# Performance work log

Measured on AMD Instinct MI355X. Metric: run time of the kernel, lower is better.

Reference implementation:

```python
import jax, jax.numpy as jnp
import numpy as np

N = 262144   # faces = edges = vertices
E = 2000000  # connections per bipartite edge set
W = 32       # out_width


def _linear_block(x, w, b):
    # LinearBlock(in, out) with defaults -> Linear + LeakyReLU(0.01)
    return jax.nn.leaky_relu(x @ w + b)


def _bip_res_mr_conv(x_src, x_dst, e, w, b):
    # diffs = x_dst[e1] - x_src[e0]; scatter_max over dst; MLP(cat) residual
    diffs = x_dst[e[1]] - x_src[e[0]]                       # [E, W]
    maxes = jax.ops.segment_max(diffs, e[1], num_segments=x_dst.shape[0])
    # torch_scatter.scatter_max fills empty slots with 0
    maxes = jnp.where(jnp.isfinite(maxes), maxes, 0.0)
    h = _linear_block(jnp.concatenate([x_dst, maxes], axis=1), w, b)
    return x_dst + h


def setup_inputs() -> dict:
    key = jax.random.key(0)
    ks = jax.random.split(key, 16)
    inp = {
        "x_f": jax.random.normal(ks[0], (N, 4), dtype=jnp.float32),
        "x_e": jax.random.normal(ks[1], (N, 6), dtype=jnp.float32),
        "x_v": jax.random.normal(ks[2], (N, 3), dtype=jnp.float32),
        "e_fe": jax.random.randint(ks[3], (2, E), 0, N),
        "e_ev": jax.random.randint(ks[4], (2, E), 0, N),
        "e_ef": jax.random.randint(ks[5], (2, E), 0, N),
        "e_ve": jax.random.randint(ks[6], (2, E), 0, N),
    }
    def lin(k, cin, cout):
        s = 1.0 / np.sqrt(cin)
        kw, kb = jax.random.split(k)
        return (jax.random.uniform(kw, (cin, cout), minval=-s, maxval=s, dtype=jnp.float32),
                jax.random.uniform(kb, (cout,), minval=-s, maxval=s, dtype=jnp.float32))
    inp["wf"], inp["bf"] = lin(ks[7], 4, W)
    inp["we"], inp["be"] = lin(ks[8], 6, W)
    inp["wv"], inp["bv"] = lin(ks[9], 3, W)
    inp["w_f2e"], inp["b_f2e"] = lin(ks[10], 2 * W, W)
    inp["w_e2v"], inp["b_e2v"] = lin(ks[11], 2 * W, W)   # E2V conv
    return inp


def reference(x_f, x_e, x_v, e_fe, e_ev, e_ef, e_ve,
              wf, bf, we, be, wv, bv, w_f2e, b_f2e, w_e2v, b_e2v):
    x_f = _linear_block(x_f, wf, bf)
    x_e = _linear_block(x_e, we, be)
    x_v = _linear_block(x_v, wv, bv)
    # NB: original forward reuses self.F2E weights for three convs
    x_e = _bip_res_mr_conv(x_f, x_e, e_fe, w_f2e, b_f2e)
    x_v = _bip_res_mr_conv(x_e, x_v, e_ev, w_e2v, b_e2v)
    x_f = _bip_res_mr_conv(x_e, x_f, e_ef, w_f2e, b_f2e)
    x_e = _bip_res_mr_conv(x_v, x_e, e_ve, w_f2e, b_f2e)
    return (x_f, x_e, x_v)
```

## Files before the change

kernel.cpp:

```cpp
#include <hip/hip_runtime.h>
#include <math.h>

#define N_NODES 262144
#define NE      2000000
#define W_OUT   32

#define NBINS          2048
#define BIN_SHIFT      7
#define NODES_PER_BIN  128
#define CAP            1200
#define EPT            16

__device__ __forceinline__ float lrelu(float x) { return x >= 0.f ? x : 0.01f * x; }

__device__ __forceinline__ unsigned fmin_key(float f) {
    unsigned u = __float_as_uint(f);
    return (u & 0x80000000u) ? ~u : (u | 0x80000000u);
}
__device__ __forceinline__ float fmin_unkey(unsigned u) {
    return __uint_as_float((u & 0x80000000u) ? (u ^ 0x80000000u) : ~u);
}

template<int K>
__global__ void proj_kernel(const float* __restrict__ x, const float* __restrict__ w,
                            const float* __restrict__ b, float* __restrict__ out) {
    __shared__ float wl[K * 32];
    __shared__ float xl[8 * K];
    int t = threadIdx.x;
    for (int i = t; i < K * 32; i += 256) wl[i] = w[i];
    int nbase = blockIdx.x * 8;
    for (int i = t; i < 8 * K; i += 256) xl[i] = x[nbase * K + i];
    __syncthreads();
    int j = t & 31, ln = t >> 5;
    float acc = b[j];
#pragma unroll
    for (int k = 0; k < K; ++k) acc += xl[ln * K + k] * wl[k * 32 + j];
    out[nbase * 32 + t] = lrelu(acc);
}

__global__ void bin_pass(const int* __restrict__ e0, const int* __restrict__ e1,
                         int* __restrict__ gcur, unsigned int* __restrict__ buckets) {
    __shared__ unsigned int hist[NBINS];
    __shared__ unsigned int lcur[NBINS];
    __shared__ unsigned int gbase[NBINS];
    int t = threadIdx.x;
    for (int i = t; i < NBINS; i += 256) hist[i] = 0;
    __syncthreads();
    long base = (long)blockIdx.x * (256 * EPT);
    for (int k = 0; k < EPT; ++k) {
        long i = base + k * 256 + t;
        if (i < NE) atomicAdd(&hist[((unsigned)e1[i]) >> BIN_SHIFT], 1u);
    }
    __syncthreads();
    for (int i = t; i < NBINS; i += 256) {
        gbase[i] = atomicAdd((unsigned int*)&gcur[i], hist[i]);
        lcur[i] = 0;
    }
    __syncthreads();
    for (int k = 0; k < EPT; ++k) {
        long i = base + k * 256 + t;
        if (i < NE) {
            unsigned d = (unsigned)e1[i];
            unsigned s = (unsigned)e0[i];
            unsigned bin = d >> BIN_SHIFT;
            unsigned pos = gbase[bin] + atomicAdd(&lcur[bin], 1u);
            if (pos < CAP)
                buckets[(size_t)bin * CAP + pos] =
                    ((d & (NODES_PER_BIN - 1u)) << 18) | s;
        }
    }
}

__global__ __launch_bounds__(256)
void binreduce4(const int* __restrict__ gcur, const unsigned int* __restrict__ buckets,
                const float* __restrict__ src, const float* __restrict__ dst,
                const float* __restrict__ w, const float* __restrict__ b,
                float* __restrict__ out) {
    __shared__ unsigned int mxu[(NODES_PER_BIN + 1) * 32];
    __shared__ float wl[64 * 32];
    __shared__ __align__(16) float xmat[8][4][64];
    int t = threadIdx.x;
    int bin = blockIdx.x;
    int hw = t >> 5, c = t & 31;

    uint4* m4 = (uint4*)mxu;
    for (int i = t; i < (NODES_PER_BIN + 1) * 32 / 4; i += 256)
        m4[i] = make_uint4(0xFFFFFFFFu, 0xFFFFFFFFu, 0xFFFFFFFFu, 0xFFFFFFFFu);
    for (int i = t; i < 64 * 32; i += 256) wl[i] = w[i];
    __syncthreads();

    int nb = min(gcur[bin], CAP);
    const unsigned int* bk = buckets + (size_t)bin * CAP;
    const unsigned SENT = (unsigned)NODES_PER_BIN << 18;
    for (int cbase = hw * 32; cbase < nb; cbase += 256) {
        int idx = cbase + c;
        unsigned ent = (idx < nb) ? bk[idx] : SENT;
#pragma unroll
        for (int k0 = 0; k0 < 32; k0 += 8) {
            float v[8];
            unsigned nd[8];
#pragma unroll
            for (int j = 0; j < 8; ++j) {
                unsigned e = __shfl(ent, k0 + j, 32);
                nd[j] = e >> 18;
                v[j] = src[(size_t)(e & 0x3FFFFu) * 32 + c];
            }
#pragma unroll
            for (int j = 0; j < 8; ++j)
                atomicMin(&mxu[nd[j] * 32 + c], fmin_key(v[j]));
        }
    }
    __syncthreads();

    float bc = b[c];
    size_t gb = (size_t)bin * NODES_PER_BIN;
    for (int grp = 0; grp < 4; ++grp) {
        int n0 = hw * 16 + grp * 4;
#pragma unroll
        for (int g = 0; g < 4; ++g) {
            int node = n0 + g;
            float dv = dst[(gb + node) * 32 + c];
            unsigned mu = mxu[node * 32 + c];
            float mx = (mu == 0xFFFFFFFFu) ? 0.0f : (dv - fmin_unkey(mu));
            xmat[hw][g][c] = dv;
            xmat[hw][g][32 + c] = mx;
        }
        __threadfence_block();

        float acc[4];
#pragma unroll
        for (int g = 0; g < 4; ++g) acc[g] = bc;

#pragma unroll 4
        for (int k4 = 0; k4 < 16; ++k4) {
            float w0 = wl[(k4 * 4 + 0) * 32 + c];
            float w1 = wl[(k4 * 4 + 1) * 32 + c];
            float w2 = wl[(k4 * 4 + 2) * 32 + c];
            float w3 = wl[(k4 * 4 + 3) * 32 + c];
#pragma unroll
            for (int g = 0; g < 4; ++g) {
                float4 xv = ((const float4*)xmat[hw][g])[k4];
                acc[g] += xv.x * w0 + xv.y * w1 + xv.z * w2 + xv.w * w3;
            }
        }
#pragma unroll
        for (int g = 0; g < 4; ++g) {
            float dv = xmat[hw][g][c];
            out[(gb + n0 + g) * 32 + c] = dv + lrelu(acc[g]);
        }
        __threadfence_block();
    }
}

extern "C" void kernel_launch(void* const* d_in, const int* in_sizes, int n_in,
                              void* d_out, int out_size, void* d_ws, size_t ws_size,
                              hipStream_t stream) {
    const float* x_f  = (const float*)d_in[0];
    const float* x_e  = (const float*)d_in[1];
    const float* x_v  = (const float*)d_in[2];
    const int*   e_fe = (const int*)d_in[3];
    const int*   e_ev = (const int*)d_in[4];
    const int*   e_ef = (const int*)d_in[5];
    const int*   e_ve = (const int*)d_in[6];
    const float* wf    = (const float*)d_in[7];
    const float* bf    = (const float*)d_in[8];
    const float* we    = (const float*)d_in[9];
    const float* be    = (const float*)d_in[10];
    const float* wv    = (const float*)d_in[11];
    const float* bv    = (const float*)d_in[12];
    const float* w_f2e = (const float*)d_in[13];
    const float* b_f2e = (const float*)d_in[14];
    const float* w_e2v = (const float*)d_in[15];
    const float* b_e2v = (const float*)d_in[16];

    float* of = (float*)d_out;
    float* oe = of + (size_t)N_NODES * W_OUT;
    float* ov = oe + (size_t)N_NODES * W_OUT;

    const int NW = N_NODES * W_OUT;

    float*        xe1     = (float*)d_ws;
    unsigned int* buckets = (unsigned int*)(xe1 + NW);
    int*          gcur4   = (int*)(buckets + (size_t)NBINS * CAP);

    dim3 blk(256);
    const int bgrid = (NE + 256 * EPT - 1) / (256 * EPT);

    hipMemsetAsync(gcur4, 0, 4 * NBINS * sizeof(int), stream);

    proj_kernel<4><<<N_NODES / 8, blk, 0, stream>>>(x_f, wf, bf, of);
    proj_kernel<6><<<N_NODES / 8, blk, 0, stream>>>(x_e, we, be, oe);
    proj_kernel<3><<<N_NODES / 8, blk, 0, stream>>>(x_v, wv, bv, ov);

    int conv_id = 0;
    auto conv = [&](const float* src, const float* dstb, const int* e,
                    const float* w, const float* bias, float* out) {
        int* gcur = gcur4 + conv_id * NBINS;
        ++conv_id;
        bin_pass<<<bgrid, blk, 0, stream>>>(e, e + NE, gcur, buckets);
        binreduce4<<<NBINS, blk, 0, stream>>>(gcur, buckets, src, dstb, w, bias, out);
    };

    conv(of,  oe,  e_fe, w_f2e, b_f2e, xe1);
    conv(xe1, ov,  e_ev, w_e2v, b_e2v, ov);
    conv(xe1, of,  e_ef, w_f2e, b_f2e, of);
    conv(ov,  xe1, e_ve, w_f2e, b_f2e, oe);
}
```

Before: 509.3 us.

## Vectorize edge binning loads and gather src rows as float4 with padded LDS

The binning pass now reads edge indices as int4, four per thread per step, in place of scalar loads. The reduce kernel uses 64-lane wavefronts: 8 lanes cooperatively gather one 128-byte src row as float4. The shared max table is padded to 33 words per row to cut LDS bank conflicts on the atomicMin updates. The MLP epilogue processes 2 nodes per group instead of 4, which lowers register use. In exchange, each lane issues four LDS atomics per load, and within a bin the order in which edges are bucketed changes.

```diff
diff --git a/kernel.cpp b/kernel.cpp
--- a/kernel.cpp
+++ b/kernel.cpp
@@ -9,7 +9,8 @@
 #define BIN_SHIFT      7
 #define NODES_PER_BIN  128
 #define CAP            1200
-#define EPT            16
+#define MROW           33
+#define MXU_DW         (((NODES_PER_BIN + 1) * MROW + 3) & ~3)
 
 __device__ __forceinline__ float lrelu(float x) { return x >= 0.f ? x : 0.01f * x; }
 
@@ -38,18 +39,28 @@
     out[nbase * 32 + t] = lrelu(acc);
 }
 
-__global__ void bin_pass(const int* __restrict__ e0, const int* __restrict__ e1,
-                         int* __restrict__ gcur, unsigned int* __restrict__ buckets) {
+__global__ __launch_bounds__(256)
+void bin_pass2(const int* __restrict__ e0, const int* __restrict__ e1,
+               int* __restrict__ gcur, unsigned int* __restrict__ buckets) {
     __shared__ unsigned int hist[NBINS];
     __shared__ unsigned int lcur[NBINS];
     __shared__ unsigned int gbase[NBINS];
     int t = threadIdx.x;
     for (int i = t; i < NBINS; i += 256) hist[i] = 0;
     __syncthreads();
-    long base = (long)blockIdx.x * (256 * EPT);
-    for (int k = 0; k < EPT; ++k) {
-        long i = base + k * 256 + t;
-        if (i < NE) atomicAdd(&hist[((unsigned)e1[i]) >> BIN_SHIFT], 1u);
+
+    int q0 = blockIdx.x * 1024 + t;
+    int4 d4[4];
+#pragma unroll
+    for (int k = 0; k < 4; ++k) {
+        int q = q0 + k * 256;
+        if (q * 4 < NE) {
+            d4[k] = ((const int4*)e1)[q];
+            atomicAdd(&hist[((unsigned)d4[k].x) >> BIN_SHIFT], 1u);
+            atomicAdd(&hist[((unsigned)d4[k].y) >> BIN_SHIFT], 1u);
+            atomicAdd(&hist[((unsigned)d4[k].z) >> BIN_SHIFT], 1u);
+            atomicAdd(&hist[((unsigned)d4[k].w) >> BIN_SHIFT], 1u);
+        }
     }
     __syncthreads();
     for (int i = t; i < NBINS; i += 256) {
@@ -57,34 +68,39 @@
         lcur[i] = 0;
     }
     __syncthreads();
-    for (int k = 0; k < EPT; ++k) {
-        long i = base + k * 256 + t;
-        if (i < NE) {
-            unsigned d = (unsigned)e1[i];
-            unsigned s = (unsigned)e0[i];
-            unsigned bin = d >> BIN_SHIFT;
-            unsigned pos = gbase[bin] + atomicAdd(&lcur[bin], 1u);
-            if (pos < CAP)
-                buckets[(size_t)bin * CAP + pos] =
-                    ((d & (NODES_PER_BIN - 1u)) << 18) | s;
+#pragma unroll
+    for (int k = 0; k < 4; ++k) {
+        int q = q0 + k * 256;
+        if (q * 4 < NE) {
+            int4 s4 = ((const int4*)e0)[q];
+            const int ds[4] = {d4[k].x, d4[k].y, d4[k].z, d4[k].w};
+            const int ss[4] = {s4.x, s4.y, s4.z, s4.w};
+#pragma unroll
+            for (int j = 0; j < 4; ++j) {
+                unsigned d = (unsigned)ds[j];
+                unsigned bin = d >> BIN_SHIFT;
+                unsigned pos = gbase[bin] + atomicAdd(&lcur[bin], 1u);
+                if (pos < CAP)
+                    buckets[(size_t)bin * CAP + pos] =
+                        ((d & (NODES_PER_BIN - 1u)) << 18) | (unsigned)ss[j];
+            }
         }
     }
 }
 
 __global__ __launch_bounds__(256)
-void binreduce4(const int* __restrict__ gcur, const unsigned int* __restrict__ buckets,
+void binreduce5(const int* __restrict__ gcur, const unsigned int* __restrict__ buckets,
                 const float* __restrict__ src, const float* __restrict__ dst,
                 const float* __restrict__ w, const float* __restrict__ b,
                 float* __restrict__ out) {
-    __shared__ unsigned int mxu[(NODES_PER_BIN + 1) * 32];
+    __shared__ unsigned int mxu[MXU_DW];
     __shared__ float wl[64 * 32];
-    __shared__ __align__(16) float xmat[8][4][64];
+    __shared__ __align__(16) float xmat[8][2][64];
     int t = threadIdx.x;
     int bin = blockIdx.x;
-    int hw = t >> 5, c = t & 31;
 
     uint4* m4 = (uint4*)mxu;
-    for (int i = t; i < (NODES_PER_BIN + 1) * 32 / 4; i += 256)
+    for (int i = t; i < MXU_DW / 4; i += 256)
         m4[i] = make_uint4(0xFFFFFFFFu, 0xFFFFFFFFu, 0xFFFFFFFFu, 0xFFFFFFFFu);
     for (int i = t; i < 64 * 32; i += 256) wl[i] = w[i];
     __syncthreads();
@@ -92,62 +108,57 @@
     int nb = min(gcur[bin], CAP);
     const unsigned int* bk = buckets + (size_t)bin * CAP;
     const unsigned SENT = (unsigned)NODES_PER_BIN << 18;
-    for (int cbase = hw * 32; cbase < nb; cbase += 256) {
-        int idx = cbase + c;
+    int l = t & 63, wv = t >> 6;
+    int g = l >> 3, q = l & 7;
+    for (int cb = wv * 64; cb < nb; cb += 256) {
+        int idx = cb + l;
         unsigned ent = (idx < nb) ? bk[idx] : SENT;
 #pragma unroll
-        for (int k0 = 0; k0 < 32; k0 += 8) {
-            float v[8];
-            unsigned nd[8];
-#pragma unroll
-            for (int j = 0; j < 8; ++j) {
-                unsigned e = __shfl(ent, k0 + j, 32);
-                nd[j] = e >> 18;
-                v[j] = src[(size_t)(e & 0x3FFFFu) * 32 + c];
-            }
-#pragma unroll
-            for (int j = 0; j < 8; ++j)
-                atomicMin(&mxu[nd[j] * 32 + c], fmin_key(v[j]));
-        }
-    }
-    __syncthreads();
-
+        for (int bq = 0; bq < 8; ++bq) {
+            unsigned e = __shfl(ent, bq * 8 + g, 64);
+            unsigned nd = e >> 18;
+            float4 v = *(const float4*)&src[(size_t)(e & 0x3FFFFu) * 32 + q * 4];
+            unsigned base = nd * MROW + q * 4;
+            atomicMin(&mxu[base + 0], fmin_key(v.x));
+            atomicMin(&mxu[base + 1], fmin_key(v.y));
+            atomicMin(&mxu[base + 2], fmin_key(v.z));
+            atomicMin(&mxu[base + 3], fmin_key(v.w));
+        }
+    }
+    __syncthreads();
+
+    int hw = t >> 5, c = t & 31;
     float bc = b[c];
     size_t gb = (size_t)bin * NODES_PER_BIN;
-    for (int grp = 0; grp < 4; ++grp) {
-        int n0 = hw * 16 + grp * 4;
-#pragma unroll
-        for (int g = 0; g < 4; ++g) {
-            int node = n0 + g;
+    for (int grp = 0; grp < 8; ++grp) {
+        int n0 = hw * 16 + grp * 2;
+#pragma unroll
+        for (int gg = 0; gg < 2; ++gg) {
+            int node = n0 + gg;
             float dv = dst[(gb + node) * 32 + c];
-            unsigned mu = mxu[node * 32 + c];
+            unsigned mu = mxu[node * MROW + c];
             float mx = (mu == 0xFFFFFFFFu) ? 0.0f : (dv - fmin_unkey(mu));
-            xmat[hw][g][c] = dv;
-            xmat[hw][g][32 + c] = mx;
+            xmat[hw][gg][c] = dv;
+            xmat[hw][gg][32 + c] = mx;
         }
         __threadfence_block();
 
-        float acc[4];
-#pragma unroll
-        for (int g = 0; g < 4; ++g) acc[g] = bc;
-
+        float acc0 = bc, acc1 = bc;
 #pragma unroll 4
         for (int k4 = 0; k4 < 16; ++k4) {
             float w0 = wl[(k4 * 4 + 0) * 32 + c];
             float w1 = wl[(k4 * 4 + 1) * 32 + c];
             float w2 = wl[(k4 * 4 + 2) * 32 + c];
             float w3 = wl[(k4 * 4 + 3) * 32 + c];
-#pragma unroll
-            for (int g = 0; g < 4; ++g) {
-                float4 xv = ((const float4*)xmat[hw][g])[k4];
-                acc[g] += xv.x * w0 + xv.y * w1 + xv.z * w2 + xv.w * w3;
-            }
-        }
-#pragma unroll
-        for (int g = 0; g < 4; ++g) {
-            float dv = xmat[hw][g][c];
-            out[(gb + n0 + g) * 32 + c] = dv + lrelu(acc[g]);
-        }
+            float4 x0 = ((const float4*)xmat[hw][0])[k4];
+            float4 x1 = ((const float4*)xmat[hw][1])[k4];
+            acc0 += x0.x * w0 + x0.y * w1 + x0.z * w2 + x0.w * w3;
+            acc1 += x1.x * w0 + x1.y * w1 + x1.z * w2 + x1.w * w3;
+        }
+        float dv0 = xmat[hw][0][c];
+        float dv1 = xmat[hw][1][c];
+        out[(gb + n0 + 0) * 32 + c] = dv0 + lrelu(acc0);
+        out[(gb + n0 + 1) * 32 + c] = dv1 + lrelu(acc1);
         __threadfence_block();
     }
 }
@@ -184,7 +195,7 @@
     int*          gcur4   = (int*)(buckets + (size_t)NBINS * CAP);
 
     dim3 blk(256);
-    const int bgrid = (NE + 256 * EPT - 1) / (256 * EPT);
+    const int bgrid = (NE + 4095) / 4096;
 
     hipMemsetAsync(gcur4, 0, 4 * NBINS * sizeof(int), stream);
 
@@ -197,8 +208,8 @@
                     const float* w, const float* bias, float* out) {
         int* gcur = gcur4 + conv_id * NBINS;
         ++conv_id;
-        bin_pass<<<bgrid, blk, 0, stream>>>(e, e + NE, gcur, buckets);
-        binreduce4<<<NBINS, blk, 0, stream>>>(gcur, buckets, src, dstb, w, bias, out);
+        bin_pass2<<<bgrid, blk, 0, stream>>>(e, e + NE, gcur, buckets);
+        binreduce5<<<NBINS, blk, 0, stream>>>(gcur, buckets, src, dstb, w, bias, out);
     };
 
     conv(of,  oe,  e_fe, w_f2e, b_f2e, xe1);
```

New measurement: 508.7 us. About the same (-0.1%).
